# Kernel tuning notes

Hardware: AMD Instinct MI355X
Metric: run time of the kernel (lower is better)

The kernel has to match this reference:

```python
import jax, jax.numpy as jnp
import numpy as np

CK = 64  # key channels, used for the 1/sqrt(ck) scale


def setup_inputs() -> dict:
    key = jax.random.key(0)
    ks = jax.random.split(key, 9)
    B, C, D, H, W = 2, 64, 20, 20, 20
    ck = cv = co = 64
    s = 0.02
    return {
        "x": jax.random.normal(ks[0], (B, C, D, H, W), dtype=jnp.float32),
        "wq": jax.random.normal(ks[1], (ck, C), dtype=jnp.float32) * s,
        "bq": jax.random.normal(ks[2], (ck,), dtype=jnp.float32) * s,
        "wk": jax.random.normal(ks[3], (ck, C), dtype=jnp.float32) * s,
        "bk": jax.random.normal(ks[4], (ck,), dtype=jnp.float32) * s,
        "wv": jax.random.normal(ks[5], (cv, C), dtype=jnp.float32) * s,
        "bv": jax.random.normal(ks[6], (cv,), dtype=jnp.float32) * s,
        "wo": jax.random.normal(ks[7], (co, cv), dtype=jnp.float32) * s,
        "bo": jax.random.normal(ks[8], (co,), dtype=jnp.float32) * s,
    }


def reference(x, wq, bq, wk, bk, wv, bv, wo, bo):
    B, C, D, H, W = x.shape
    ck = wq.shape[0]
    cv = wv.shape[0]
    xf = x.reshape(B, C, -1)  # (B, C, N) with N = D*H*W
    # 1x1x1 convs == per-voxel channel matmuls
    q = jnp.einsum('kc,bcn->bnk', wq, xf) + bq           # (B, N, ck) queries (already transposed)
    k = jnp.einsum('kc,bcn->bkn', wk, xf) + bk[:, None]  # (B, ck, N) keys
    v = jnp.einsum('vc,bcn->bnv', wv, xf) + bv           # (B, N, cv) values (transposed)
    scale = 1.0 / jnp.sqrt(jnp.asarray(CK, dtype=x.dtype))
    attn = jax.nn.softmax(jnp.einsum('bnk,bkm->bnm', q, k) * scale, axis=-1)  # (B, N, N)
    # dropout is identity in eval mode
    out = jnp.einsum('bnm,bmv->bnv', attn, v)  # (B, N, cv)
    # faithful to torch: .view(batch, cv, d, h, w) reinterprets memory, no transpose
    out = out.reshape(B, cv, D, H, W)
    out = jnp.einsum('oc,bcdhw->bodhw', wo, out) + bo[None, :, None, None, None]
    return out
```

## Files before the change

kernel.cpp:

```cpp
#include <hip/hip_runtime.h>
#include <hip/hip_bf16.h>

typedef __bf16 bf16_t;
typedef __bf16 bf16x8 __attribute__((ext_vector_type(8)));
typedef float f32x4 __attribute__((ext_vector_type(4)));
typedef float f32x16 __attribute__((ext_vector_type(16)));
typedef unsigned uint2v __attribute__((ext_vector_type(2)));

#define NV 8000
#define QB 125

#define GLOAD_LDS16(src, dst) \
    __builtin_amdgcn_global_load_lds((const __attribute__((address_space(1))) void*)(src), \
                                     (__attribute__((address_space(3))) void*)(dst), 16, 0, 0)

__device__ __forceinline__ bf16x8 cvt_bf16x8(const float* __restrict__ p) {
    float4 a = *reinterpret_cast<const float4*>(p);
    float4 b = *reinterpret_cast<const float4*>(p + 4);
    bf16x8 r;
    r[0] = (bf16_t)a.x; r[1] = (bf16_t)a.y; r[2] = (bf16_t)a.z; r[3] = (bf16_t)a.w;
    r[4] = (bf16_t)b.x; r[5] = (bf16_t)b.y; r[6] = (bf16_t)b.z; r[7] = (bf16_t)b.w;
    return r;
}

__device__ __forceinline__ unsigned pack2(float a, float b) {
    union { bf16_t h[2]; unsigned u; } x;
    x.h[0] = (bf16_t)a; x.h[1] = (bf16_t)b;
    return x.u;
}

__device__ __forceinline__ int sigma_of(int n) {
    int c = n / 125, a = n - 125 * c;
    return a * 64 + c;
}

__global__ __launch_bounds__(256) void qkv_kernel(
    const float* __restrict__ x,
    const float* __restrict__ wq, const float* __restrict__ bq,
    const float* __restrict__ wk, const float* __restrict__ bk,
    const float* __restrict__ wv, const float* __restrict__ bv,
    bf16_t* __restrict__ Q, bf16_t* __restrict__ Kr, bf16_t* __restrict__ Vt)
{
    __shared__ __align__(16) char xb[16 * 128];

    const int tid = threadIdx.x;
    const int b  = blockIdx.x / 500;
    const int n0 = (blockIdx.x % 500) * 16;

    {
        int c = tid >> 2, seg = tid & 3;
        float4 v4 = *reinterpret_cast<const float4*>(&x[((size_t)b * 64 + c) * NV + n0 + seg * 4]);
        #pragma unroll
        for (int j = 0; j < 4; ++j) {
            int vx = seg * 4 + j;
            *reinterpret_cast<bf16_t*>(xb + vx * 128 + ((c * 2) ^ ((vx & 7) << 4))) =
                (bf16_t)((&v4.x)[j]);
        }
    }
    __syncthreads();

    const int w  = tid >> 6;
    const int lane = tid & 63;
    const int g  = lane >> 4;
    const int lr = lane & 15;

    const bf16x8 xa0 = *reinterpret_cast<const bf16x8*>(
        xb + lr * 128 + ((16 * g) ^ ((lr & 7) << 4)));
    const bf16x8 xa1 = *reinterpret_cast<const bf16x8*>(
        xb + lr * 128 + ((64 + 16 * g) ^ ((lr & 7) << 4)));

    const f32x4 zero4 = {0.f, 0.f, 0.f, 0.f};
    const float QSCALE = 0.125f * 1.44269504088896f;
    const int kout = w * 16 + lr;

    {
        bf16x8 wb0 = cvt_bf16x8(wq + kout * 64 + 8 * g);
        bf16x8 wb1 = cvt_bf16x8(wq + kout * 64 + 32 + 8 * g);
        f32x4 acc = __builtin_amdgcn_mfma_f32_16x16x32_bf16(xa0, wb0, zero4, 0, 0, 0);
        acc = __builtin_amdgcn_mfma_f32_16x16x32_bf16(xa1, wb1, acc, 0, 0, 0);
        const float bias = bq[kout];
        #pragma unroll
        for (int j = 0; j < 4; ++j) {
            const int sig = sigma_of(n0 + 4 * g + j);
            Q[((size_t)b * NV + sig) * 64 + kout] = (bf16_t)((acc[j] + bias) * QSCALE);
        }
    }
    {
        bf16x8 wb0 = cvt_bf16x8(wk + kout * 64 + 8 * g);
        bf16x8 wb1 = cvt_bf16x8(wk + kout * 64 + 32 + 8 * g);
        f32x4 acc = __builtin_amdgcn_mfma_f32_16x16x32_bf16(xa0, wb0, zero4, 0, 0, 0);
        acc = __builtin_amdgcn_mfma_f32_16x16x32_bf16(xa1, wb1, acc, 0, 0, 0);
        const float bias = bk[kout];
        #pragma unroll
        for (int j = 0; j < 4; ++j)
            Kr[((size_t)b * NV + n0 + 4 * g + j) * 64 + kout] = (bf16_t)(acc[j] + bias);
    }
    {
        bf16x8 wb0 = cvt_bf16x8(wv + kout * 64 + 8 * g);
        bf16x8 wb1 = cvt_bf16x8(wv + kout * 64 + 32 + 8 * g);
        f32x4 acc = __builtin_amdgcn_mfma_f32_16x16x32_bf16(xa0, wb0, zero4, 0, 0, 0);
        acc = __builtin_amdgcn_mfma_f32_16x16x32_bf16(xa1, wb1, acc, 0, 0, 0);
        const float bias = bv[kout];
        union { uint2 u2; bf16_t h[4]; } pk;
        #pragma unroll
        for (int j = 0; j < 4; ++j) pk.h[j] = (bf16_t)(acc[j] + bias);
        *reinterpret_cast<uint2*>(&Vt[((size_t)b * 64 + kout) * NV + n0 + 4 * g]) = pk.u2;
    }
}

template<int S>
__global__ __launch_bounds__(256) void attn_kernel(
    const bf16_t* __restrict__ Q, const bf16_t* __restrict__ Kr,
    const bf16_t* __restrict__ Vt, float* __restrict__ Op, float* __restrict__ ml)
{
    __shared__ __align__(16) char kt[2][8192];
    __shared__ __align__(16) char vt[2][8192];

    const int tid  = threadIdx.x;
    const int s    = blockIdx.x % S;
    const int rem  = blockIdx.x / S;
    const int b    = rem / 63;
    const int qb   = rem % 63;
    const int q0   = qb * 128;
    const int t0   = (125 * s) / S;
    const int t1   = (125 * (s + 1)) / S;
    const int w    = tid >> 6;
    const int lane = tid & 63;
    const int lo   = lane & 31;
    const int hi   = lane >> 5;

    const int q  = q0 + w * 32 + lo;
    const int qc = q < NV ? q : NV - 1;

    bf16x8 bq[4];
    {
        const bf16_t* qrow = Q + ((size_t)b * NV + qc) * 64 + hi * 8;
        #pragma unroll
        for (int kk = 0; kk < 4; ++kk)
            bq[kk] = *reinterpret_cast<const bf16x8*>(qrow + kk * 16);
    }

    const char* kp = (const char*)(Kr + (size_t)b * NV * 64);
    const char* vp = (const char*)(Vt + (size_t)b * 64 * NV);

    f32x16 acco[2]; acco[0] = f32x16{}; acco[1] = f32x16{};
    float m = -1e30f, l = 0.f;

    #define STAGE_TILE(m0, kdst, vdst)                                                   \
        _Pragma("unroll")                                                                \
        for (int rr = 0; rr < 2; ++rr) {                                                 \
            const int gk = w + 4 * rr;                                                   \
            const int kb_ = gk >> 2, kk_ = gk & 3;                                       \
            GLOAD_LDS16(kp + (size_t)((m0) + kb_ * 32 + lo) * 128 + kk_ * 32 + hi * 16,  \
                        (kdst) + gk * 1024);                                             \
            const int ks_ = gk >> 1, vb_ = gk & 1;                                       \
            GLOAD_LDS16(vp + (size_t)(vb_ * 32 + lo) * (NV * 2)                          \
                           + (size_t)((m0) + ks_ * 16 + hi * 8) * 2,                     \
                        (vdst) + gk * 1024);                                             \
        }

    STAGE_TILE(t0 * 64, kt[0], vt[0]);

    for (int t = t0; t < t1; ++t) {
        const int cur = (t - t0) & 1;
        __syncthreads();
        if (t + 1 < t1) {
            STAGE_TILE((t + 1) * 64, kt[cur ^ 1], vt[cur ^ 1]);
        }

        const char* ktb = kt[cur];
        f32x16 sa[2];
        #pragma unroll
        for (int kb = 0; kb < 2; ++kb) {
            f32x16 acc{};
            #pragma unroll
            for (int kk = 0; kk < 4; ++kk) {
                const bf16x8 ka = *reinterpret_cast<const bf16x8*>(
                    ktb + ((kb * 4 + kk) * 64 + lane) * 16);
                acc = __builtin_amdgcn_mfma_f32_32x32x16_bf16(ka, bq[kk], acc, 0, 0, 0);
            }
            sa[kb] = acc;
        }

        float mx;
        {
            float v8[8];
            #pragma unroll
            for (int r = 0; r < 8; ++r)
                v8[r] = fmaxf(fmaxf(sa[0][r], sa[0][r + 8]),
                              fmaxf(sa[1][r], sa[1][r + 8]));
            float v4a = fmaxf(v8[0], v8[4]), v4b = fmaxf(v8[1], v8[5]);
            float v4c = fmaxf(v8[2], v8[6]), v4d = fmaxf(v8[3], v8[7]);
            mx = fmaxf(fmaxf(v4a, v4b), fmaxf(v4c, v4d));
        }
        {
            union { float f; unsigned u; } xu; xu.f = mx;
            uint2v r = __builtin_amdgcn_permlane32_swap(xu.u, xu.u, false, false);
            union { unsigned u; float f; } po; po.u = hi ? r[0] : r[1];
            mx = fmaxf(mx, po.f);
        }

        if (__any(mx > m + 8.0f)) {
            const float mn2 = fmaxf(m, mx);
            const float corr = exp2f(m - mn2);
            m = mn2;
            l *= corr;
            acco[0] *= corr;
            acco[1] *= corr;
        }

        float ps = 0.f;
        unsigned Uw[2][4][2];
        #pragma unroll
        for (int kb = 0; kb < 2; ++kb) {
            #pragma unroll
            for (int j = 0; j < 4; ++j) {
                float p0 = exp2f(sa[kb][4 * j + 0] - m);
                float p1 = exp2f(sa[kb][4 * j + 1] - m);
                float p2 = exp2f(sa[kb][4 * j + 2] - m);
                float p3 = exp2f(sa[kb][4 * j + 3] - m);
                ps += (p0 + p1) + (p2 + p3);
                Uw[kb][j][0] = pack2(p0, p1);
                Uw[kb][j][1] = pack2(p2, p3);
            }
        }
        {
            union { float f; unsigned u; } xu; xu.f = ps;
            uint2v r = __builtin_amdgcn_permlane32_swap(xu.u, xu.u, false, false);
            union { unsigned u; float f; } po; po.u = hi ? r[0] : r[1];
            ps += po.f;
        }
        l += ps;

        const char* vtb = vt[cur];
        #pragma unroll
        for (int kb = 0; kb < 2; ++kb) {
            #pragma unroll
            for (int e = 0; e < 2; ++e) {
                uint2v r0 = __builtin_amdgcn_permlane32_swap(
                    Uw[kb][2 * e][0], Uw[kb][2 * e + 1][0], false, false);
                uint2v r1 = __builtin_amdgcn_permlane32_swap(
                    Uw[kb][2 * e][1], Uw[kb][2 * e + 1][1], false, false);
                union { unsigned u[4]; bf16x8 v; } pf;
                pf.u[0] = r0[0]; pf.u[1] = r1[0];
                pf.u[2] = r0[1]; pf.u[3] = r1[1];
                const int ks = kb * 2 + e;
                #pragma unroll
                for (int vb = 0; vb < 2; ++vb) {
                    const bf16x8 va = *reinterpret_cast<const bf16x8*>(
                        vtb + ((ks * 2 + vb) * 64 + lane) * 16);
                    acco[vb] = __builtin_amdgcn_mfma_f32_32x32x16_bf16(va, pf.v, acco[vb], 0, 0, 0);
                }
            }
        }
    }

    if (q < NV) {
        const size_t obase = ((size_t)(s * 2 + b) * NV + q) * 64;
        #pragma unroll
        for (int vb = 0; vb < 2; ++vb) {
            #pragma unroll
            for (int j = 0; j < 4; ++j) {
                f32x4 o4 = { acco[vb][4 * j + 0], acco[vb][4 * j + 1],
                             acco[vb][4 * j + 2], acco[vb][4 * j + 3] };
                *reinterpret_cast<f32x4*>(&Op[obase + vb * 32 + 8 * j + 4 * hi]) = o4;
            }
        }
        if (hi == 0) {
            float2 t2; t2.x = m; t2.y = l;
            *reinterpret_cast<float2*>(&ml[((size_t)(s * 2 + b) * NV + q) * 2]) = t2;
        }
    }
    #undef STAGE_TILE
}

template<int S>
__global__ __launch_bounds__(256) void projc_kernel(
    const float* __restrict__ Op, const float* __restrict__ ml,
    const float* __restrict__ wo, const float* __restrict__ bo,
    float* __restrict__ out)
{
    __shared__ __align__(16) char bt[64 * 128];
    __shared__ float al[64 * 8];

    const int tid = threadIdx.x;
    const int b   = blockIdx.x / 125;
    const int a   = blockIdx.x % 125;

    if (tid < 64) {
        const int row = a * 64 + tid;
        float M = -1e30f;
        #pragma unroll
        for (int s = 0; s < S; ++s)
            M = fmaxf(M, ml[((size_t)(s * 2 + b) * NV + row) * 2]);
        float L = 0.f, av[S];
        #pragma unroll
        for (int s = 0; s < S; ++s) {
            const float mm = ml[((size_t)(s * 2 + b) * NV + row) * 2];
            const float ll = ml[((size_t)(s * 2 + b) * NV + row) * 2 + 1];
            const float aa = exp2f(mm - M);
            L += ll * aa;
            av[s] = aa;
        }
        const float inv = 1.0f / L;
        #pragma unroll
        for (int s = 0; s < S; ++s) al[tid * 8 + s] = av[s] * inv;
    }
    __syncthreads();

    {
        const int c = tid >> 2, sg = tid & 3;
        f32x4 acc[4] = {{0,0,0,0},{0,0,0,0},{0,0,0,0},{0,0,0,0}};
        #pragma unroll
        for (int s = 0; s < S; ++s) {
            const float fac = al[c * 8 + s];
            const float* base = &Op[((size_t)(s * 2 + b) * NV + a * 64 + c) * 64 + sg * 16];
            #pragma unroll
            for (int qq = 0; qq < 4; ++qq)
                acc[qq] += fac * *reinterpret_cast<const f32x4*>(base + qq * 4);
        }
        #pragma unroll
        for (int qq = 0; qq < 4; ++qq) {
            #pragma unroll
            for (int j = 0; j < 4; ++j) {
                const int v = sg * 16 + qq * 4 + j;
                *reinterpret_cast<bf16_t*>(bt + v * 128 + ((c * 2) ^ ((v & 7) << 4))) =
                    (bf16_t)acc[qq][j];
            }
        }
    }
    __syncthreads();

    const int w  = tid >> 6;
    const int lane = tid & 63;
    const int g  = lane >> 4;
    const int lr = lane & 15;

    const int orow = w * 16 + lr;
    const bf16x8 wa0 = cvt_bf16x8(wo + orow * 64 + 8 * g);
    const bf16x8 wa1 = cvt_bf16x8(wo + orow * 64 + 32 + 8 * g);
    const float4 bo4 = *reinterpret_cast<const float4*>(&bo[w * 16 + 4 * g]);

    const f32x4 zero4 = {0.f, 0.f, 0.f, 0.f};
    #pragma unroll
    for (int nf = 0; nf < 4; ++nf) {
        const int rrow = nf * 16 + lr;
        const bf16x8 gb0 = *reinterpret_cast<const bf16x8*>(
            bt + rrow * 128 + ((16 * g) ^ ((rrow & 7) << 4)));
        const bf16x8 gb1 = *reinterpret_cast<const bf16x8*>(
            bt + rrow * 128 + ((64 + 16 * g) ^ ((rrow & 7) << 4)));
        f32x4 acc = __builtin_amdgcn_mfma_f32_16x16x32_bf16(wa0, gb0, zero4, 0, 0, 0);
        acc = __builtin_amdgcn_mfma_f32_16x16x32_bf16(wa1, gb1, acc, 0, 0, 0);
        #pragma unroll
        for (int j = 0; j < 4; ++j) {
            const int o = w * 16 + 4 * g + j;
            out[((size_t)b * 64 + o) * NV + a * 64 + nf * 16 + lr] = acc[j] + (&bo4.x)[j];
        }
    }
}

extern "C" void kernel_launch(void* const* d_in, const int* in_sizes, int n_in,
                              void* d_out, int out_size, void* d_ws, size_t ws_size,
                              hipStream_t stream)
{
    const float* x  = (const float*)d_in[0];
    const float* wq = (const float*)d_in[1];
    const float* bq = (const float*)d_in[2];
    const float* wk = (const float*)d_in[3];
    const float* bk = (const float*)d_in[4];
    const float* wv = (const float*)d_in[5];
    const float* bv = (const float*)d_in[6];
    const float* wo = (const float*)d_in[7];
    const float* bo = (const float*)d_in[8];
    float* out = (float*)d_out;

    char* ws = (char*)d_ws;
    bf16_t* Q  = (bf16_t*)(ws);
    bf16_t* Kr = (bf16_t*)(ws + 2048000);
    bf16_t* Vt = (bf16_t*)(ws + 4096000);

    int S = 8;
    if (ws_size < 6144000ull + 8ull * 4224000ull) S = 4;
    if (ws_size < 6144000ull + 4ull * 4224000ull) S = 2;
    if (ws_size < 6144000ull + 2ull * 4224000ull) S = 1;

    float* Op = (float*)(ws + 6144000);
    float* ml = (float*)(ws + 6144000 + (size_t)S * 4096000);

    qkv_kernel<<<dim3(2 * 500), dim3(256), 0, stream>>>(x, wq, bq, wk, bk, wv, bv, Q, Kr, Vt);

    if (S == 8) {
        attn_kernel<8><<<dim3(8 * 2 * 63), dim3(256), 0, stream>>>(Q, Kr, Vt, Op, ml);
        projc_kernel<8><<<dim3(2 * 125), dim3(256), 0, stream>>>(Op, ml, wo, bo, out);
    } else if (S == 4) {
        attn_kernel<4><<<dim3(4 * 2 * 63), dim3(256), 0, stream>>>(Q, Kr, Vt, Op, ml);
        projc_kernel<4><<<dim3(2 * 125), dim3(256), 0, stream>>>(Op, ml, wo, bo, out);
    } else if (S == 2) {
        attn_kernel<2><<<dim3(2 * 2 * 63), dim3(256), 0, stream>>>(Q, Kr, Vt, Op, ml);
        projc_kernel<2><<<dim3(2 * 125), dim3(256), 0, stream>>>(Op, ml, wo, bo, out);
    } else {
        attn_kernel<1><<<dim3(1 * 2 * 63), dim3(256), 0, stream>>>(Q, Kr, Vt, Op, ml);
        projc_kernel<1><<<dim3(2 * 125), dim3(256), 0, stream>>>(Op, ml, wo, bo, out);
    }
}
```

Baseline: 181.1 us.

## Software-pipeline attention tiles via registers, store partials in bf16, split projection blocks

The attention loop stops using direct global-to-LDS loads. It now prefetches K/V tiles into registers two tiles ahead and computes QK^T for the next tile before the softmax and PV of the current one, so memory latency and MFMA work overlap. Split partial outputs are written as bf16 instead of fp32, which halves workspace traffic between the attention and combine kernels. The projection kernel is split four ways per block to raise parallelism. In exchange, each loop iteration now has two barriers and more register pressure, and the bf16 partials lose precision.

```diff
diff --git a/kernel.cpp b/kernel.cpp
--- a/kernel.cpp
+++ b/kernel.cpp
@@ -9,10 +9,6 @@
 
 #define NV 8000
 #define QB 125
-
-#define GLOAD_LDS16(src, dst) \
-    __builtin_amdgcn_global_load_lds((const __attribute__((address_space(1))) void*)(src), \
-                                     (__attribute__((address_space(3))) void*)(dst), 16, 0, 0)
 
 __device__ __forceinline__ bf16x8 cvt_bf16x8(const float* __restrict__ p) {
     float4 a = *reinterpret_cast<const float4*>(p);
@@ -111,7 +107,7 @@
 template<int S>
 __global__ __launch_bounds__(256) void attn_kernel(
     const bf16_t* __restrict__ Q, const bf16_t* __restrict__ Kr,
-    const bf16_t* __restrict__ Vt, float* __restrict__ Op, float* __restrict__ ml)
+    const bf16_t* __restrict__ Vt, bf16_t* __restrict__ Op, float* __restrict__ ml)
 {
     __shared__ __align__(16) char kt[2][8192];
     __shared__ __align__(16) char vt[2][8192];
@@ -132,55 +128,65 @@
     const int q  = q0 + w * 32 + lo;
     const int qc = q < NV ? q : NV - 1;
 
-    bf16x8 bq[4];
+    bf16x8 bqf[4];
     {
         const bf16_t* qrow = Q + ((size_t)b * NV + qc) * 64 + hi * 8;
         #pragma unroll
         for (int kk = 0; kk < 4; ++kk)
-            bq[kk] = *reinterpret_cast<const bf16x8*>(qrow + kk * 16);
+            bqf[kk] = *reinterpret_cast<const bf16x8*>(qrow + kk * 16);
     }
 
     const char* kp = (const char*)(Kr + (size_t)b * NV * 64);
     const char* vp = (const char*)(Vt + (size_t)b * 64 * NV);
 
+    const int gk0 = w, gk1 = w + 4;
+    const size_t koff0 = (size_t)((gk0 >> 2) * 32 + lo) * 128 + (gk0 & 3) * 32 + hi * 16;
+    const size_t koff1 = (size_t)((gk1 >> 2) * 32 + lo) * 128 + (gk1 & 3) * 32 + hi * 16;
+    const size_t voff0 = (size_t)((gk0 & 1) * 32 + lo) * (NV * 2) + (size_t)((gk0 >> 1) * 16 + hi * 8) * 2;
+    const size_t voff1 = (size_t)((gk1 & 1) * 32 + lo) * (NV * 2) + (size_t)((gk1 >> 1) * 16 + hi * 8) * 2;
+    const int dst0 = gk0 * 1024 + lane * 16;
+    const int dst1 = gk1 * 1024 + lane * 16;
+
+    uint4 rk0_, rk1_, rv0_, rv1_;
+#define ATTN_GLOB(m0) do { \
+    rk0_ = *reinterpret_cast<const uint4*>(kp + (size_t)(m0) * 128 + koff0); \
+    rk1_ = *reinterpret_cast<const uint4*>(kp + (size_t)(m0) * 128 + koff1); \
+    rv0_ = *reinterpret_cast<const uint4*>(vp + (size_t)(m0) * 2 + voff0); \
+    rv1_ = *reinterpret_cast<const uint4*>(vp + (size_t)(m0) * 2 + voff1); } while (0)
+#define ATTN_DSW(bufi) do { \
+    *reinterpret_cast<uint4*>(kt[bufi] + dst0) = rk0_; \
+    *reinterpret_cast<uint4*>(kt[bufi] + dst1) = rk1_; \
+    *reinterpret_cast<uint4*>(vt[bufi] + dst0) = rv0_; \
+    *reinterpret_cast<uint4*>(vt[bufi] + dst1) = rv1_; } while (0)
+#define ATTN_QK(bufi, dst) do { \
+    const char* ktb_ = kt[bufi]; \
+    _Pragma("unroll") \
+    for (int kb = 0; kb < 2; ++kb) { \
+        f32x16 acc_{}; \
+        _Pragma("unroll") \
+        for (int kk = 0; kk < 4; ++kk) { \
+            const bf16x8 ka_ = *reinterpret_cast<const bf16x8*>( \
+                ktb_ + ((kb * 4 + kk) * 64 + lane) * 16); \
+            acc_ = __builtin_amdgcn_mfma_f32_32x32x16_bf16(ka_, bqf[kk], acc_, 0, 0, 0); \
+        } \
+        dst[kb] = acc_; } } while (0)
+
     f32x16 acco[2]; acco[0] = f32x16{}; acco[1] = f32x16{};
     float m = -1e30f, l = 0.f;
 
-    #define STAGE_TILE(m0, kdst, vdst)                                                   \
-        _Pragma("unroll")                                                                \
-        for (int rr = 0; rr < 2; ++rr) {                                                 \
-            const int gk = w + 4 * rr;                                                   \
-            const int kb_ = gk >> 2, kk_ = gk & 3;                                       \
-            GLOAD_LDS16(kp + (size_t)((m0) + kb_ * 32 + lo) * 128 + kk_ * 32 + hi * 16,  \
-                        (kdst) + gk * 1024);                                             \
-            const int ks_ = gk >> 1, vb_ = gk & 1;                                       \
-            GLOAD_LDS16(vp + (size_t)(vb_ * 32 + lo) * (NV * 2)                          \
-                           + (size_t)((m0) + ks_ * 16 + hi * 8) * 2,                     \
-                        (vdst) + gk * 1024);                                             \
-        }
-
-    STAGE_TILE(t0 * 64, kt[0], vt[0]);
+    const int nt = t1 - t0;
+    ATTN_GLOB(t0 * 64); ATTN_DSW(0);
+    if (nt > 1) { ATTN_GLOB((t0 + 1) * 64); ATTN_DSW(1); }
+    if (nt > 2) ATTN_GLOB((t0 + 2) * 64);
+    __syncthreads();
+
+    f32x16 sa[2], sa2[2];
+    ATTN_QK(0, sa);
 
     for (int t = t0; t < t1; ++t) {
-        const int cur = (t - t0) & 1;
-        __syncthreads();
-        if (t + 1 < t1) {
-            STAGE_TILE((t + 1) * 64, kt[cur ^ 1], vt[cur ^ 1]);
-        }
-
-        const char* ktb = kt[cur];
-        f32x16 sa[2];
-        #pragma unroll
-        for (int kb = 0; kb < 2; ++kb) {
-            f32x16 acc{};
-            #pragma unroll
-            for (int kk = 0; kk < 4; ++kk) {
-                const bf16x8 ka = *reinterpret_cast<const bf16x8*>(
-                    ktb + ((kb * 4 + kk) * 64 + lane) * 16);
-                acc = __builtin_amdgcn_mfma_f32_32x32x16_bf16(ka, bq[kk], acc, 0, 0, 0);
-            }
-            sa[kb] = acc;
-        }
+        const int p = (t - t0) & 1;
+
+        if (t + 1 < t1) ATTN_QK(p ^ 1, sa2);
 
         float mx;
         {
@@ -199,7 +205,6 @@
             union { unsigned u; float f; } po; po.u = hi ? r[0] : r[1];
             mx = fmaxf(mx, po.f);
         }
-
         if (__any(mx > m + 8.0f)) {
             const float mn2 = fmaxf(m, mx);
             const float corr = exp2f(m - mn2);
@@ -232,7 +237,7 @@
         }
         l += ps;
 
-        const char* vtb = vt[cur];
+        const char* vtb = vt[p];
         #pragma unroll
         for (int kb = 0; kb < 2; ++kb) {
             #pragma unroll
@@ -253,6 +258,12 @@
                 }
             }
         }
+
+        __syncthreads();
+        if (t + 2 < t1) ATTN_DSW(p);
+        __syncthreads();
+        if (t + 3 < t1) ATTN_GLOB((t + 3) * 64);
+        if (t + 1 < t1) { sa[0] = sa2[0]; sa[1] = sa2[1]; }
     }
 
     if (q < NV) {
@@ -261,9 +272,10 @@
         for (int vb = 0; vb < 2; ++vb) {
             #pragma unroll
             for (int j = 0; j < 4; ++j) {
-                f32x4 o4 = { acco[vb][4 * j + 0], acco[vb][4 * j + 1],
-                             acco[vb][4 * j + 2], acco[vb][4 * j + 3] };
-                *reinterpret_cast<f32x4*>(&Op[obase + vb * 32 + 8 * j + 4 * hi]) = o4;
+                union { uint2 u2; bf16_t h[4]; } pk;
+                #pragma unroll
+                for (int i = 0; i < 4; ++i) pk.h[i] = (bf16_t)acco[vb][4 * j + i];
+                *reinterpret_cast<uint2*>(&Op[obase + vb * 32 + 8 * j + 4 * hi]) = pk.u2;
             }
         }
         if (hi == 0) {
@@ -271,21 +283,25 @@
             *reinterpret_cast<float2*>(&ml[((size_t)(s * 2 + b) * NV + q) * 2]) = t2;
         }
     }
-    #undef STAGE_TILE
+#undef ATTN_GLOB
+#undef ATTN_DSW
+#undef ATTN_QK
 }
 
 template<int S>
 __global__ __launch_bounds__(256) void projc_kernel(
-    const float* __restrict__ Op, const float* __restrict__ ml,
+    const bf16_t* __restrict__ Op, const float* __restrict__ ml,
     const float* __restrict__ wo, const float* __restrict__ bo,
     float* __restrict__ out)
 {
-    __shared__ __align__(16) char bt[64 * 128];
+    __shared__ __align__(16) char bt[16 * 128];
     __shared__ float al[64 * 8];
 
     const int tid = threadIdx.x;
-    const int b   = blockIdx.x / 125;
-    const int a   = blockIdx.x % 125;
+    const int b   = blockIdx.x / 500;
+    const int rem = blockIdx.x % 500;
+    const int a   = rem >> 2;
+    const int nf  = rem & 3;
 
     if (tid < 64) {
         const int row = a * 64 + tid;
@@ -310,23 +326,21 @@
 
     {
         const int c = tid >> 2, sg = tid & 3;
-        f32x4 acc[4] = {{0,0,0,0},{0,0,0,0},{0,0,0,0},{0,0,0,0}};
+        f32x4 acc = {0.f, 0.f, 0.f, 0.f};
         #pragma unroll
         for (int s = 0; s < S; ++s) {
             const float fac = al[c * 8 + s];
-            const float* base = &Op[((size_t)(s * 2 + b) * NV + a * 64 + c) * 64 + sg * 16];
+            union { uint2 u2; bf16_t h[4]; } cv;
+            cv.u2 = *reinterpret_cast<const uint2*>(
+                &Op[((size_t)(s * 2 + b) * NV + a * 64 + c) * 64 + nf * 16 + sg * 4]);
             #pragma unroll
-            for (int qq = 0; qq < 4; ++qq)
-                acc[qq] += fac * *reinterpret_cast<const f32x4*>(base + qq * 4);
-        }
-        #pragma unroll
-        for (int qq = 0; qq < 4; ++qq) {
-            #pragma unroll
-            for (int j = 0; j < 4; ++j) {
-                const int v = sg * 16 + qq * 4 + j;
-                *reinterpret_cast<bf16_t*>(bt + v * 128 + ((c * 2) ^ ((v & 7) << 4))) =
-                    (bf16_t)acc[qq][j];
-            }
+            for (int j = 0; j < 4; ++j) acc[j] += fac * (float)cv.h[j];
+        }
+        #pragma unroll
+        for (int j = 0; j < 4; ++j) {
+            const int v = sg * 4 + j;
+            *reinterpret_cast<bf16_t*>(bt + v * 128 + ((c * 2) ^ ((v & 7) << 4))) =
+                (bf16_t)acc[j];
         }
     }
     __syncthreads();
@@ -342,20 +356,16 @@
     const float4 bo4 = *reinterpret_cast<const float4*>(&bo[w * 16 + 4 * g]);
 
     const f32x4 zero4 = {0.f, 0.f, 0.f, 0.f};
+    const bf16x8 gb0 = *reinterpret_cast<const bf16x8*>(
+        bt + lr * 128 + ((16 * g) ^ ((lr & 7) << 4)));
+    const bf16x8 gb1 = *reinterpret_cast<const bf16x8*>(
+        bt + lr * 128 + ((64 + 16 * g) ^ ((lr & 7) << 4)));
+    f32x4 acc = __builtin_amdgcn_mfma_f32_16x16x32_bf16(wa0, gb0, zero4, 0, 0, 0);
+    acc = __builtin_amdgcn_mfma_f32_16x16x32_bf16(wa1, gb1, acc, 0, 0, 0);
     #pragma unroll
-    for (int nf = 0; nf < 4; ++nf) {
-        const int rrow = nf * 16 + lr;
-        const bf16x8 gb0 = *reinterpret_cast<const bf16x8*>(
-            bt + rrow * 128 + ((16 * g) ^ ((rrow & 7) << 4)));
-        const bf16x8 gb1 = *reinterpret_cast<const bf16x8*>(
-            bt + rrow * 128 + ((64 + 16 * g) ^ ((rrow & 7) << 4)));
-        f32x4 acc = __builtin_amdgcn_mfma_f32_16x16x32_bf16(wa0, gb0, zero4, 0, 0, 0);
-        acc = __builtin_amdgcn_mfma_f32_16x16x32_bf16(wa1, gb1, acc, 0, 0, 0);
-        #pragma unroll
-        for (int j = 0; j < 4; ++j) {
-            const int o = w * 16 + 4 * g + j;
-            out[((size_t)b * 64 + o) * NV + a * 64 + nf * 16 + lr] = acc[j] + (&bo4.x)[j];
-        }
+    for (int j = 0; j < 4; ++j) {
+        const int o = w * 16 + 4 * g + j;
+        out[((size_t)b * 64 + o) * NV + a * 64 + nf * 16 + lr] = acc[j] + (&bo4.x)[j];
     }
 }
 
@@ -380,26 +390,26 @@
     bf16_t* Vt = (bf16_t*)(ws + 4096000);
 
     int S = 8;
-    if (ws_size < 6144000ull + 8ull * 4224000ull) S = 4;
-    if (ws_size < 6144000ull + 4ull * 4224000ull) S = 2;
-    if (ws_size < 6144000ull + 2ull * 4224000ull) S = 1;
-
-    float* Op = (float*)(ws + 6144000);
-    float* ml = (float*)(ws + 6144000 + (size_t)S * 4096000);
+    if (ws_size < 6144000ull + 8ull * 2176000ull) S = 4;
+    if (ws_size < 6144000ull + 4ull * 2176000ull) S = 2;
+    if (ws_size < 6144000ull + 2ull * 2176000ull) S = 1;
+
+    bf16_t* Op = (bf16_t*)(ws + 6144000);
+    float*  ml = (float*)(ws + 6144000 + (size_t)S * 2048000);
 
     qkv_kernel<<<dim3(2 * 500), dim3(256), 0, stream>>>(x, wq, bq, wk, bk, wv, bv, Q, Kr, Vt);
 
     if (S == 8) {
         attn_kernel<8><<<dim3(8 * 2 * 63), dim3(256), 0, stream>>>(Q, Kr, Vt, Op, ml);
-        projc_kernel<8><<<dim3(2 * 125), dim3(256), 0, stream>>>(Op, ml, wo, bo, out);
+        projc_kernel<8><<<dim3(2 * 500), dim3(256), 0, stream>>>(Op, ml, wo, bo, out);
     } else if (S == 4) {
         attn_kernel<4><<<dim3(4 * 2 * 63), dim3(256), 0, stream>>>(Q, Kr, Vt, Op, ml);
-        projc_kernel<4><<<dim3(2 * 125), dim3(256), 0, stream>>>(Op, ml, wo, bo, out);
+        projc_kernel<4><<<dim3(2 * 500), dim3(256), 0, stream>>>(Op, ml, wo, bo, out);
     } else if (S == 2) {
         attn_kernel<2><<<dim3(2 * 2 * 63), dim3(256), 0, stream>>>(Q, Kr, Vt, Op, ml);
-        projc_kernel<2><<<dim3(2 * 125), dim3(256), 0, stream>>>(Op, ml, wo, bo, out);
+        projc_kernel<2><<<dim3(2 * 500), dim3(256), 0, stream>>>(Op, ml, wo, bo, out);
     } else {
         attn_kernel<1><<<dim3(1 * 2 * 63), dim3(256), 0, stream>>>(Q, Kr, Vt, Op, ml);
-        projc_kernel<1><<<dim3(2 * 125), dim3(256), 0, stream>>>(Op, ml, wo, bo, out);
-    }
-}
+        projc_kernel<1><<<dim3(2 * 500), dim3(256), 0, stream>>>(Op, ml, wo, bo, out);
+    }
+}
```

Result: faster. 175.6 us (-3.0%).
